# Optimization experiments

Hardware: AMD Instinct MI355X
Metric: run time of the kernel (lower is better)

## Reference

```python
import jax, jax.numpy as jnp
import numpy as np

IN_CH = 128
OUT_CH = 128
INPUT_LEN = 512
KERNEL = 8
STRIDE = 1
OUT_LEN = (INPUT_LEN - KERNEL) // STRIDE + 1  # 505
BATCH = 64


def setup_inputs() -> dict:
    key = jax.random.key(0)
    kx, kw, kb = jax.random.split(key, 3)
    x = jax.random.normal(kx, (BATCH, IN_CH, INPUT_LEN), dtype=jnp.float32)
    weight = jax.random.normal(kw, (OUT_LEN, OUT_CH, IN_CH, KERNEL), dtype=jnp.float32)
    bias = jax.random.normal(kb, (OUT_CH, OUT_LEN), dtype=jnp.float32)
    return {"x": x, "weight": weight, "bias": bias}


def reference(x, weight, bias):
    # unfold: gather sliding windows -> [b, i, l_out, k]
    idx = jnp.arange(OUT_LEN)[:, None] * STRIDE + jnp.arange(KERNEL)[None, :]  # [l, k]
    x_unf = x[:, :, idx]  # [b, i, l, k]
    # per-position independent GEMM: 'blik,loik->bol' with x permuted to bilk
    out = jnp.einsum('bilk,loik->bol', x_unf, weight)
    out = out + bias[None, :, :]
    return out
```

## Files before the change

kernel.cpp:

```cpp
#include <hip/hip_runtime.h>
#include <hip/hip_bf16.h>

#define BATCH 64
#define IN_CH 128
#define ILEN  512
#define OLEN  505
#define OCH   128
#define KDIM  1024
#define BK    64
#define NCHK  16
#define NWG   (OLEN * 2)

typedef float f32x4  __attribute__((ext_vector_type(4)));
typedef short bf16x8 __attribute__((ext_vector_type(8)));

__device__ __forceinline__ short f2bf(float f) {
  union { __hip_bfloat16 h; short s; } u;
  u.h = __float2bfloat16(f);
  return u.s;
}

template <bool USE_TMP>
__global__ __launch_bounds__(256, 3) void lc1d_main(
    const float* __restrict__ x, const float* __restrict__ w,
    const float* __restrict__ bias, float* __restrict__ outp) {
  {
  }
  const int orig = blockIdx.x;
  const int xcd = orig & 7, idx = orig >> 3;
  const int q = NWG / 8, rr = NWG % 8;
  const int wg = (xcd < rr ? xcd * (q + 1) : rr * (q + 1) + (xcd - rr) * q) + idx;
  const int l  = wg >> 1;
  const int oh = wg & 1;

  const int tid  = threadIdx.x;
  const int lane = tid & 63;
  const int wn   = tid >> 6;
  const int r    = lane & 15;
  const int h    = lane >> 4;

  __shared__ float Bs[2][BK * 64];
  __shared__ short As[2][BK * 64];

  f32x4 acc[4];
#pragma unroll
  for (int m = 0; m < 4; ++m) acc[m] = (f32x4){0.f, 0.f, 0.f, 0.f};

  const float* __restrict__ wl =
      w + (size_t)l * (OCH * KDIM) + (size_t)oh * 64 * KDIM;

  const int so  = tid >> 4;
  const int sc  = tid & 15;
  const int ssw = ((so & 7) << 1) | ((so >> 3) & 1);

  const int kk  = tid & 63;
  const int tb  = tid >> 6;
  const int il  = kk >> 3;
  const int kof = kk & 7;

  float aa[16];

  auto loadA = [&](int kc) {
    const float* xb = x + (size_t)(kc * 8 + il) * ILEN + l + kof;
#pragma unroll
    for (int it = 0; it < 16; ++it)
      aa[it] = xb[(size_t)(it * 4 + tb) * (IN_CH * ILEN)];
  };
  auto writeA = [&](int buf) {
#pragma unroll
    for (int it = 0; it < 16; ++it) {
      const int b = it * 4 + tb;
      As[buf][b * 64 + (kk ^ ((b & 7) << 3))] = f2bf(aa[it]);
    }
  };
  auto stageB = [&](int buf, int kc) {
#pragma unroll
    for (int it = 0; it < 4; ++it) {
      const int ob = it * 16 + so;
      const float* src = wl + (size_t)ob * KDIM + kc * BK + (sc ^ ssw) * 4;
      __builtin_amdgcn_global_load_lds(
          (const __attribute__((address_space(1))) void*)src,
          (__attribute__((address_space(3))) void*)&Bs[buf][ob * 64 + sc * 4],
          16, 0, 0);
    }
  };

  const int rsw = ((r & 7) << 1) | ((r >> 3) & 1);
  auto compute = [&](int cur) {
    const int ob = wn * 16 + r;
#pragma unroll
    for (int ks = 0; ks < 2; ++ks) {
      const int c0 = ks * 8 + h * 2;
      const f32x4 blo = *reinterpret_cast<const f32x4*>(
          &Bs[cur][ob * 64 + ((c0) ^ rsw) * 4]);
      const f32x4 bhi = *reinterpret_cast<const f32x4*>(
          &Bs[cur][ob * 64 + ((c0 + 1) ^ rsw) * 4]);
      bf16x8 bfr;
#pragma unroll
      for (int j = 0; j < 4; ++j) {
        bfr[j]     = f2bf(blo[j]);
        bfr[4 + j] = f2bf(bhi[j]);
      }
#pragma unroll
      for (int mt = 0; mt < 4; ++mt) {
        const int b = mt * 16 + r;
        const bf16x8 afr = *reinterpret_cast<const bf16x8*>(
            &As[cur][b * 64 + ((ks * 32 + h * 8) ^ ((b & 7) << 3))]);
        acc[mt] = __builtin_amdgcn_mfma_f32_16x16x32_bf16(afr, bfr, acc[mt], 0, 0, 0);
      }
    }
  };

  loadA(0);
  stageB(0, 0);
  writeA(0);
  __syncthreads();

  for (int kc = 0; kc < NCHK; ++kc) {
    const int cur = kc & 1, nxt = cur ^ 1;
    if (kc + 1 < NCHK) {
      loadA(kc + 1);
      stageB(nxt, kc + 1);
    }
    compute(cur);
    if (kc + 1 < NCHK) writeA(nxt);
    __syncthreads();
  }

  const int og = oh * 64 + wn * 16 + r;
  if (USE_TMP) {
    float* t = outp + (size_t)l * (BATCH * OCH) + og;
#pragma unroll
    for (int mt = 0; mt < 4; ++mt)
#pragma unroll
      for (int j = 0; j < 4; ++j) {
        const int b = mt * 16 + h * 4 + j;
        t[(size_t)b * OCH] = acc[mt][j];
      }
  } else {
    const float bv = bias[og * OLEN + l];
#pragma unroll
    for (int mt = 0; mt < 4; ++mt)
#pragma unroll
      for (int j = 0; j < 4; ++j) {
        const int b = mt * 16 + h * 4 + j;
        outp[(size_t)b * (OCH * OLEN) + (size_t)og * OLEN + l] = acc[mt][j] + bv;
      }
  }
}

__global__ __launch_bounds__(256) void lc1d_tr(const float* __restrict__ tmp,
                                               const float* __restrict__ bias,
                                               float* __restrict__ out) {
  const int l0  = blockIdx.x * 64;
  const int bo0 = blockIdx.y * 64;
  const int tid = threadIdx.x;
  __shared__ float t[64][65];

  const int boj = tid & 63, lq = tid >> 6;
#pragma unroll
  for (int rr = 0; rr < 16; ++rr) {
    const int li = rr * 4 + lq;
    const int l  = l0 + li;
    if (l < OLEN) t[li][boj] = tmp[(size_t)l * (BATCH * OCH) + bo0 + boj];
  }
  __syncthreads();
  const int lj = tid & 63, bq = tid >> 6;
  const int l  = l0 + lj;
#pragma unroll
  for (int rr = 0; rr < 16; ++rr) {
    const int bl = rr * 4 + bq;
    const int bo = bo0 + bl;
    if (l < OLEN) {
      const int oc = bo & (OCH - 1);
      out[(size_t)bo * OLEN + l] = t[lj][bl] + bias[oc * OLEN + l];
    }
  }
}

extern "C" void kernel_launch(void* const* d_in, const int* in_sizes, int n_in,
                              void* d_out, int out_size, void* d_ws, size_t ws_size,
                              hipStream_t stream) {
  const float* x    = (const float*)d_in[0];
  const float* w    = (const float*)d_in[1];
  const float* bias = (const float*)d_in[2];
  float* out        = (float*)d_out;

  const size_t need = (size_t)OLEN * BATCH * OCH * sizeof(float);
  if (ws_size >= need) {
    float* tmp = (float*)d_ws;
    lc1d_main<true><<<dim3(NWG), 256, 0, stream>>>(x, w, bias, tmp);
    lc1d_tr<<<dim3(8, 128), 256, 0, stream>>>(tmp, bias, out);
  } else {
    lc1d_main<false><<<dim3(NWG), 256, 0, stream>>>(x, w, bias, out);
  }
}
```

Measured before the change: 110.5 us.

## Deepen main-kernel pipeline to prefetch two chunks ahead with manual waitcnt barriers

```diff
diff --git a/kernel.cpp b/kernel.cpp
--- a/kernel.cpp
+++ b/kernel.cpp
@@ -21,15 +21,13 @@
 }
 
 template <bool USE_TMP>
-__global__ __launch_bounds__(256, 3) void lc1d_main(
+__global__ __launch_bounds__(256, 2) void lc1d_main(
     const float* __restrict__ x, const float* __restrict__ w,
     const float* __restrict__ bias, float* __restrict__ outp) {
-  {
-  }
   const int orig = blockIdx.x;
   const int xcd = orig & 7, idx = orig >> 3;
-  const int q = NWG / 8, rr = NWG % 8;
-  const int wg = (xcd < rr ? xcd * (q + 1) : rr * (q + 1) + (xcd - rr) * q) + idx;
+  const int q = NWG / 8, rm = NWG % 8;
+  const int wg = (xcd < rm ? xcd * (q + 1) : rm * (q + 1) + (xcd - rm) * q) + idx;
   const int l  = wg >> 1;
   const int oh = wg & 1;
 
@@ -39,7 +37,7 @@
   const int r    = lane & 15;
   const int h    = lane >> 4;
 
-  __shared__ float Bs[2][BK * 64];
+  __shared__ float Bs[3][BK * 64];
   __shared__ short As[2][BK * 64];
 
   f32x4 acc[4];
@@ -58,15 +56,15 @@
   const int il  = kk >> 3;
   const int kof = kk & 7;
 
-  float aa[16];
-
-  auto loadA = [&](int kc) {
+  float aa0[16], aa1[16];
+
+  auto loadA = [&](float (&aa)[16], int kc) {
     const float* xb = x + (size_t)(kc * 8 + il) * ILEN + l + kof;
 #pragma unroll
     for (int it = 0; it < 16; ++it)
       aa[it] = xb[(size_t)(it * 4 + tb) * (IN_CH * ILEN)];
   };
-  auto writeA = [&](int buf) {
+  auto writeA = [&](const float (&aa)[16], int buf) {
 #pragma unroll
     for (int it = 0; it < 16; ++it) {
       const int b = it * 4 + tb;
@@ -86,15 +84,15 @@
   };
 
   const int rsw = ((r & 7) << 1) | ((r >> 3) & 1);
-  auto compute = [&](int cur) {
+  auto compute = [&](int bB, int bA) {
     const int ob = wn * 16 + r;
 #pragma unroll
     for (int ks = 0; ks < 2; ++ks) {
       const int c0 = ks * 8 + h * 2;
       const f32x4 blo = *reinterpret_cast<const f32x4*>(
-          &Bs[cur][ob * 64 + ((c0) ^ rsw) * 4]);
+          &Bs[bB][ob * 64 + ((c0) ^ rsw) * 4]);
       const f32x4 bhi = *reinterpret_cast<const f32x4*>(
-          &Bs[cur][ob * 64 + ((c0 + 1) ^ rsw) * 4]);
+          &Bs[bB][ob * 64 + ((c0 + 1) ^ rsw) * 4]);
       bf16x8 bfr;
 #pragma unroll
       for (int j = 0; j < 4; ++j) {
@@ -105,26 +103,41 @@
       for (int mt = 0; mt < 4; ++mt) {
         const int b = mt * 16 + r;
         const bf16x8 afr = *reinterpret_cast<const bf16x8*>(
-            &As[cur][b * 64 + ((ks * 32 + h * 8) ^ ((b & 7) << 3))]);
+            &As[bA][b * 64 + ((ks * 32 + h * 8) ^ ((b & 7) << 3))]);
         acc[mt] = __builtin_amdgcn_mfma_f32_16x16x32_bf16(afr, bfr, acc[mt], 0, 0, 0);
       }
     }
   };
 
-  loadA(0);
+  loadA(aa0, 0);
   stageB(0, 0);
-  writeA(0);
-  __syncthreads();
-
+  writeA(aa0, 0);
+  loadA(aa1, 1);
+  stageB(1, 1);
+  asm volatile("s_waitcnt vmcnt(20) lgkmcnt(0)" ::: "memory");
+  __builtin_amdgcn_sched_barrier(0);
+  __builtin_amdgcn_s_barrier();
+  __builtin_amdgcn_sched_barrier(0);
+
+#pragma unroll
   for (int kc = 0; kc < NCHK; ++kc) {
-    const int cur = kc & 1, nxt = cur ^ 1;
+    if (kc + 2 < NCHK) {
+      if ((kc & 1) == 0) loadA(aa0, kc + 2); else loadA(aa1, kc + 2);
+      stageB((kc + 2) % 3, kc + 2);
+    }
+    __builtin_amdgcn_sched_barrier(0);
+    compute(kc % 3, kc & 1);
     if (kc + 1 < NCHK) {
-      loadA(kc + 1);
-      stageB(nxt, kc + 1);
-    }
-    compute(cur);
-    if (kc + 1 < NCHK) writeA(nxt);
-    __syncthreads();
+      if ((kc & 1) == 0) writeA(aa1, 1); else writeA(aa0, 0);
+      if (kc + 2 < NCHK) {
+        asm volatile("s_waitcnt vmcnt(20) lgkmcnt(0)" ::: "memory");
+      } else {
+        asm volatile("s_waitcnt vmcnt(0) lgkmcnt(0)" ::: "memory");
+      }
+      __builtin_amdgcn_sched_barrier(0);
+      __builtin_amdgcn_s_barrier();
+      __builtin_amdgcn_sched_barrier(0);
+    }
   }
 
   const int og = oh * 64 + wn * 16 + r;
```

Result: no change. 109.3 us (-1.1%).
